# Kernel tuning notes

Measured on AMD Instinct MI355X. Metric: run time of the kernel, lower is better.

Reference implementation:

```python
import jax, jax.numpy as jnp
import numpy as np

PI = jnp.pi
NB_FRAMES = 2


def _axis_angle_to_R(r):
    # r: [..., 3] axis-angle -> rotation matrix [..., 3, 3] (Rodrigues)
    eps = 1e-8
    theta = jnp.sqrt(jnp.sum(r * r, axis=-1, keepdims=True))  # [...,1]
    k = r / jnp.maximum(theta, eps)
    kx, ky, kz = k[..., 0], k[..., 1], k[..., 2]
    zero = jnp.zeros_like(kx)
    K = jnp.stack([
        jnp.stack([zero, -kz, ky], axis=-1),
        jnp.stack([kz, zero, -kx], axis=-1),
        jnp.stack([-ky, kx, zero], axis=-1),
    ], axis=-2)  # [...,3,3]
    I = jnp.eye(3, dtype=r.dtype)
    s = jnp.sin(theta)[..., None]
    c = jnp.cos(theta)[..., None]
    return I + s * K + (1.0 - c) * (K @ K)


def _equirec_dirs(h, w, dtype):
    # unit viewing directions of an equirectangular grid, [h, w, 3]
    lon = ((jnp.arange(w, dtype=dtype) + 0.5) / w * 2.0 - 1.0) * PI
    lat = -((jnp.arange(h, dtype=dtype) + 0.5) / h * 2.0 - 1.0) * (0.5 * PI)
    LON, LAT = jnp.meshgrid(lon, lat)  # [h, w]
    dx = jnp.cos(LAT) * jnp.sin(LON)
    dy = jnp.sin(LAT)
    dz = jnp.cos(LAT) * jnp.cos(LON)
    return jnp.stack([dx, dy, dz], axis=-1)


def _grid_sample(img, grid):
    # img: [B,C,H,W]; grid: [B,Hg,Wg,2] in [-1,1] (x,y); bilinear,
    # align_corners=True, zero padding (matches F.grid_sample defaults)
    B, C, H, W = img.shape
    x = (grid[..., 0] + 1.0) * 0.5 * (W - 1)
    y = (grid[..., 1] + 1.0) * 0.5 * (H - 1)
    x0 = jnp.floor(x)
    y0 = jnp.floor(y)
    x1 = x0 + 1.0
    y1 = y0 + 1.0
    img_flat = img.reshape(B, C, H * W)

    def gather(xi, yi):
        valid = (xi >= 0) & (xi <= W - 1) & (yi >= 0) & (yi <= H - 1)
        xc = jnp.clip(xi, 0, W - 1).astype(jnp.int32)
        yc = jnp.clip(yi, 0, H - 1).astype(jnp.int32)
        idx = (yc * W + xc).reshape(B, 1, -1)
        v = jnp.take_along_axis(img_flat, idx, axis=2).reshape(B, C, *xi.shape[1:])
        return v * valid[:, None].astype(img.dtype)

    wa = ((x1 - x) * (y1 - y))[:, None]
    wb = ((x1 - x) * (y - y0))[:, None]
    wc = ((x - x0) * (y1 - y))[:, None]
    wd = ((x - x0) * (y - y0))[:, None]
    return (gather(x0, y0) * wa + gather(x0, y1) * wb +
            gather(x1, y0) * wc + gather(x1, y1) * wd)


def _area_down(x, s):
    # F.interpolate(mode='area') with integer factor == average pooling
    if s == 1:
        return x
    B, C, H, W = x.shape
    return x.reshape(B, C, H // s, s, W // s, s).mean(axis=(3, 5))


def _photometric_loss(ref_rgb, depths, masks, tgts, pose):
    R = _axis_angle_to_R(pose[..., 3:])      # [B, nb, 3, 3]
    t = pose[..., :3]                         # [B, nb, 3]
    loss = jnp.zeros((), dtype=ref_rgb.dtype)
    for i, (d, m) in enumerate(zip(depths, masks)):
        s = 2 ** i
        h, w = d.shape[2], d.shape[3]
        rr = _area_down(ref_rgb, s)                       # [B,3,h,w]
        tg = [_area_down(tr, s) for tr in tgts]
        dirs = _equirec_dirs(h, w, ref_rgb.dtype)         # [h,w,3]
        xyz = d[:, 0, :, :, None] * dirs[None]            # [B,h,w,3]
        # pose transform: pts = R @ xyz + t  -> [B,h,w,nb,3]
        pts = jnp.einsum('bnij,bhwj->bhwni', R, xyz) + t[:, None, None]
        norm = jnp.sqrt(jnp.sum(pts * pts, axis=-1))
        lon = jnp.arctan2(pts[..., 0], pts[..., 2])
        lat = jnp.arcsin(jnp.clip(pts[..., 1] / jnp.maximum(norm, 1e-8), -1.0, 1.0))
        X = lon / PI                  # [B,h,w,nb]
        Y = lat / (0.5 * PI)
        for j in range(NB_FRAMES):
            coord = jnp.stack([X[..., j], Y[..., j]], axis=-1)  # [B,h,w,2]
            wf = _grid_sample(tg[j], coord)                     # [B,3,h,w]
            loss = loss + jnp.mean(m[:, j:j + 1] * jnp.abs(rr - wf))
    return loss


def setup_inputs() -> dict:
    key = jax.random.key(0)
    ks = jax.random.split(key, 16)
    B, H, W = 8, 512, 1024
    inp = {'ref_rgb': jax.random.uniform(ks[0], (B, 3, H, W), jnp.float32)}
    for i in range(4):
        h, w = H // (2 ** i), W // (2 ** i)
        inp[f'ref_depth{i}'] = jax.random.uniform(ks[1 + i], (B, 1, h, w), jnp.float32)
        inp[f'exp_mask{i}'] = jax.random.uniform(ks[5 + i], (B, NB_FRAMES, h, w), jnp.float32)
    inp['tgt_rgb0'] = jax.random.uniform(ks[9], (B, 3, H, W), jnp.float32)
    inp['tgt_rgb1'] = jax.random.uniform(ks[10], (B, 3, H, W), jnp.float32)
    inp['pose'] = jax.random.normal(ks[11], (B, NB_FRAMES, 6), jnp.float32)
    return inp


def reference(ref_rgb, ref_depth0, ref_depth1, ref_depth2, ref_depth3,
              exp_mask0, exp_mask1, exp_mask2, exp_mask3,
              tgt_rgb0, tgt_rgb1, pose):
    depths = [ref_depth0, ref_depth1, ref_depth2, ref_depth3]
    masks = [exp_mask0, exp_mask1, exp_mask2, exp_mask3]
    tgts = [tgt_rgb0, tgt_rgb1]
    return _photometric_loss(ref_rgb, depths, masks, tgts, pose)
```

## Files before the change

kernel.cpp:

```cpp
#include <hip/hip_runtime.h>
#include <hip/hip_fp16.h>
#include <math.h>

#define PI_F 3.14159265358979323846f

__device__ inline float fast_atan2f(float y, float x) {
    float ax = fabsf(x), ay = fabsf(y);
    float mx = fmaxf(ax, ay);
    float mn = fminf(ax, ay);
    float a = __fdividef(mn, fmaxf(mx, 1e-30f));
    float s = a * a;
    float r = fmaf(s, fmaf(s, fmaf(s, fmaf(s, fmaf(s, -0.01172120f, 0.05265332f),
                   -0.11643287f), 0.19354346f), -0.33262347f), 0.99997726f);
    r = r * a;
    if (ay > ax) r = 1.57079632679f - r;
    if (x < 0.0f) r = PI_F - r;
    return copysignf(r, y);
}

__device__ inline void make_Rt_to(const float* __restrict__ pose, int bn, float* __restrict__ o) {
    const float* p = pose + bn * 6;
    float tx = p[0], ty = p[1], tz = p[2];
    float rx = p[3], ry = p[4], rz = p[5];
    float theta = sqrtf(rx * rx + ry * ry + rz * rz);
    float inv = __fdividef(1.0f, fmaxf(theta, 1e-8f));
    float kx = rx * inv, ky = ry * inv, kz = rz * inv;
    float s, c;
    __sincosf(theta, &s, &c);
    float oc = 1.0f - c;
    o[0] = 1.0f - oc * (ky * ky + kz * kz);
    o[1] = -s * kz + oc * kx * ky;
    o[2] =  s * ky + oc * kx * kz;
    o[3] =  s * kz + oc * kx * ky;
    o[4] = 1.0f - oc * (kx * kx + kz * kz);
    o[5] = -s * kx + oc * ky * kz;
    o[6] = -s * ky + oc * kx * kz;
    o[7] =  s * kx + oc * ky * kz;
    o[8] = 1.0f - oc * (kx * kx + ky * ky);
    o[9] = tx; o[10] = ty; o[11] = tz;
}

__device__ inline uint2 pack_px(float r, float g, float b) {
    __half2 a = __floats2half2_rn(r, g);
    __half2 c = __floats2half2_rn(b, 0.0f);
    uint2 u;
    u.x = *(const unsigned int*)&a;
    u.y = *(const unsigned int*)&c;
    return u;
}
__device__ inline float3 unpack_px(uint2 u) {
    __half2 a = *(const __half2*)&u.x;
    __half2 c = *(const __half2*)&u.y;
    float2 f = __half22float2(a);
    return make_float3(f.x, f.y, __low2float(c));
}

__global__ __launch_bounds__(256) void prep_kernel(
    const float* __restrict__ ref, const float* __restrict__ tgt0, const float* __restrict__ tgt1,
    uint2* __restrict__ packF,
    uint2* __restrict__ pL1t, uint2* __restrict__ pL2t, uint2* __restrict__ pL3t,
    uint2* __restrict__ pL1r, uint2* __restrict__ pL2r, uint2* __restrict__ pL3r)
{
    int bid = blockIdx.x;
    int band = bid & 63;
    int ib = bid >> 6;
    int b = ib & 7;
    int i = ib >> 3;
    const float* img = (i == 0) ? ref : (i == 1) ? tgt0 : tgt1;
    int t = threadIdx.x;
    int x4 = t << 2;
    int y0 = band << 3;
    int q = (i - 1) * 8 + b;

    float l1v[4][2][3];
#pragma unroll
    for (int p = 0; p < 4; ++p) {
        float4 a[3], bb[3];
#pragma unroll
        for (int c = 0; c < 3; ++c) {
            const float* pl = img + ((size_t)(b * 3 + c) << 19);
            a[c]  = *(const float4*)(pl + ((y0 + 2 * p) << 10) + x4);
            bb[c] = *(const float4*)(pl + ((y0 + 2 * p + 1) << 10) + x4);
        }
        if (i > 0) {
            uint2* o = packF + ((size_t)q << 19) + ((y0 + 2 * p) << 10) + x4;
            uint2 p0 = pack_px(a[0].x, a[1].x, a[2].x);
            uint2 p1 = pack_px(a[0].y, a[1].y, a[2].y);
            uint2 p2 = pack_px(a[0].z, a[1].z, a[2].z);
            uint2 p3 = pack_px(a[0].w, a[1].w, a[2].w);
            uint4 v0; v0.x = p0.x; v0.y = p0.y; v0.z = p1.x; v0.w = p1.y;
            uint4 v1; v1.x = p2.x; v1.y = p2.y; v1.z = p3.x; v1.w = p3.y;
            *(uint4*)o = v0;
            *(uint4*)(o + 2) = v1;
            uint2* o2 = o + (1 << 10);
            p0 = pack_px(bb[0].x, bb[1].x, bb[2].x);
            p1 = pack_px(bb[0].y, bb[1].y, bb[2].y);
            p2 = pack_px(bb[0].z, bb[1].z, bb[2].z);
            p3 = pack_px(bb[0].w, bb[1].w, bb[2].w);
            v0.x = p0.x; v0.y = p0.y; v0.z = p1.x; v0.w = p1.y;
            v1.x = p2.x; v1.y = p2.y; v1.z = p3.x; v1.w = p3.y;
            *(uint4*)o2 = v0;
            *(uint4*)(o2 + 2) = v1;
        }
#pragma unroll
        for (int c = 0; c < 3; ++c) {
            l1v[p][0][c] = (a[c].x + a[c].y + bb[c].x + bb[c].y) * 0.25f;
            l1v[p][1][c] = (a[c].z + a[c].w + bb[c].z + bb[c].w) * 0.25f;
        }
        uint2 q0 = pack_px(l1v[p][0][0], l1v[p][0][1], l1v[p][0][2]);
        uint2 q1 = pack_px(l1v[p][1][0], l1v[p][1][1], l1v[p][1][2]);
        uint4 v; v.x = q0.x; v.y = q0.y; v.z = q1.x; v.w = q1.y;
        uint2* d1 = ((i == 0) ? pL1r + ((size_t)b << 17) : pL1t + ((size_t)q << 17))
                    + (((band << 2) + p) << 9) + (t << 1);
        *(uint4*)d1 = v;
    }
    float l2v[2][3];
#pragma unroll
    for (int pr = 0; pr < 2; ++pr) {
#pragma unroll
        for (int c = 0; c < 3; ++c)
            l2v[pr][c] = (l1v[2 * pr][0][c] + l1v[2 * pr][1][c] +
                          l1v[2 * pr + 1][0][c] + l1v[2 * pr + 1][1][c]) * 0.25f;
        uint2* d2 = ((i == 0) ? pL2r + ((size_t)b << 15) : pL2t + ((size_t)q << 15))
                    + (((band << 1) + pr) << 8) + t;
        *d2 = pack_px(l2v[pr][0], l2v[pr][1], l2v[pr][2]);
    }
    float l3[3];
#pragma unroll
    for (int c = 0; c < 3; ++c) {
        float s = l2v[0][c] + l2v[1][c];
        l3[c] = (s + __shfl_xor(s, 1)) * 0.25f;
    }
    if ((t & 1) == 0) {
        uint2* d3 = ((i == 0) ? pL3r + ((size_t)b << 13) : pL3t + ((size_t)q << 13))
                    + (band << 7) + (t >> 1);
        *d3 = pack_px(l3[0], l3[1], l3[2]);
    }
}

template <int SH>
__device__ inline float photo_scale4(int bidl, int tid,
                                     const float* __restrict__ rrF,
                                     const uint2* __restrict__ rrP,
                                     const float* __restrict__ depth,
                                     const float* __restrict__ mask,
                                     const uint2* __restrict__ tg,
                                     const float* __restrict__ pose,
                                     float* __restrict__ ldsRt) {
    constexpr int h = 512 >> SH;
    constexpr int w = 1024 >> SH;
    constexpr int LOG2W = 10 - SH;
    constexpr int LP = 19 - 2 * SH;
    constexpr float inv_count = 1.0f / (8.0f * 3.0f * h * w);

    int lidx = ((bidl << 8) + tid) << 2;
    int b = lidx >> LP;
    if (tid < 2) make_Rt_to(pose, b * 2 + tid, ldsRt + tid * 12);
    __syncthreads();

    int x0 = lidx & (w - 1);
    int y = (lidx >> LOG2W) & (h - 1);
    int pix = (y << LOG2W) + x0;

    float lat = -(((float)y + 0.5f) * (2.0f / (float)h) - 1.0f) * (0.5f * PI_F);
    float slat = __sinf(lat), clat = __cosf(lat);

    float4 dep4 = *(const float4*)(depth + ((size_t)b << LP) + pix);
    float dp[4] = {dep4.x, dep4.y, dep4.z, dep4.w};
    float rcv[4][3];
    if constexpr (SH == 0) {
#pragma unroll
        for (int c = 0; c < 3; ++c) {
            float4 rv = *(const float4*)(rrF + ((size_t)(b * 3 + c) << LP) + pix);
            rcv[0][c] = rv.x; rcv[1][c] = rv.y; rcv[2][c] = rv.z; rcv[3][c] = rv.w;
        }
    } else {
        const uint2* rp = rrP + ((size_t)b << LP) + pix;
        uint4 u01 = *(const uint4*)rp;
        uint4 u23 = *(const uint4*)(rp + 2);
        uint2 e0; e0.x = u01.x; e0.y = u01.y;
        uint2 e1; e1.x = u01.z; e1.y = u01.w;
        uint2 e2; e2.x = u23.x; e2.y = u23.y;
        uint2 e3; e3.x = u23.z; e3.y = u23.w;
        float3 f0 = unpack_px(e0), f1 = unpack_px(e1), f2 = unpack_px(e2), f3 = unpack_px(e3);
        rcv[0][0] = f0.x; rcv[0][1] = f0.y; rcv[0][2] = f0.z;
        rcv[1][0] = f1.x; rcv[1][1] = f1.y; rcv[1][2] = f1.z;
        rcv[2][0] = f2.x; rcv[2][1] = f2.y; rcv[2][2] = f2.z;
        rcv[3][0] = f3.x; rcv[3][1] = f3.y; rcv[3][2] = f3.z;
    }
    float m4[2][4];
#pragma unroll
    for (int n = 0; n < 2; ++n) {
        float4 mv = *(const float4*)(mask + ((size_t)(b * 2 + n) << LP) + pix);
        m4[n][0] = mv.x; m4[n][1] = mv.y; m4[n][2] = mv.z; m4[n][3] = mv.w;
    }

    float acc = 0.0f;
#pragma unroll
    for (int i = 0; i < 4; ++i) {
        float lon = (((float)(x0 + i) + 0.5f) * (2.0f / (float)w) - 1.0f) * PI_F;
        float sl = __sinf(lon), cl = __cosf(lon);
        float X = dp[i] * clat * sl, Y = dp[i] * slat, Z = dp[i] * clat * cl;
#pragma unroll
        for (int n = 0; n < 2; ++n) {
            const float* R = ldsRt + n * 12;
            float px = R[0] * X + R[1] * Y + R[2] * Z + R[9];
            float py = R[3] * X + R[4] * Y + R[5] * Z + R[10];
            float pz = R[6] * X + R[7] * Y + R[8] * Z + R[11];
            float rxz = sqrtf(px * px + pz * pz);
            float lon2 = fast_atan2f(px, pz);
            float lat2 = fast_atan2f(py, rxz);
            float gx = (lon2 * (1.0f / PI_F) + 1.0f) * 0.5f * (float)(w - 1);
            float gy = (lat2 * (2.0f / PI_F) + 1.0f) * 0.5f * (float)(h - 1);
            float x0f = floorf(gx), y0f = floorf(gy);
            float fx = gx - x0f, fy = gy - y0f;
            float wa = (1.0f - fx) * (1.0f - fy);
            float wb = (1.0f - fx) * fy;
            float wc = fx * (1.0f - fy);
            float wd = fx * fy;
            bool vx0 = (x0f >= 0.0f) && (x0f <= (float)(w - 1));
            bool vx1 = (x0f >= -1.0f) && (x0f <= (float)(w - 2));
            bool vy0 = (y0f >= 0.0f) && (y0f <= (float)(h - 1));
            bool vy1 = (y0f >= -1.0f) && (y0f <= (float)(h - 2));
            int xi0 = (int)fminf(fmaxf(x0f, 0.0f), (float)(w - 1));
            int xi1 = (int)fminf(fmaxf(x0f + 1.0f, 0.0f), (float)(w - 1));
            int yi0 = (int)fminf(fmaxf(y0f, 0.0f), (float)(h - 1));
            int yi1 = (int)fminf(fmaxf(y0f + 1.0f, 0.0f), (float)(h - 1));
            float waf = (vx0 && vy0) ? wa : 0.0f;
            float wbf = (vx0 && vy1) ? wb : 0.0f;
            float wcf = (vx1 && vy0) ? wc : 0.0f;
            float wdf = (vx1 && vy1) ? wd : 0.0f;

            const uint2* plane = tg + ((size_t)(n * 8 + b) << LP);
            uint2 ua = plane[(yi0 << LOG2W) + xi0];
            uint2 ub = plane[(yi1 << LOG2W) + xi0];
            uint2 uc = plane[(yi0 << LOG2W) + xi1];
            uint2 ud = plane[(yi1 << LOG2W) + xi1];
            float3 ta = unpack_px(ua), tb = unpack_px(ub), tc = unpack_px(uc), td = unpack_px(ud);

            float m = m4[n][i];
            float v0 = waf * ta.x + wbf * tb.x + wcf * tc.x + wdf * td.x;
            float v1 = waf * ta.y + wbf * tb.y + wcf * tc.y + wdf * td.y;
            float v2 = waf * ta.z + wbf * tb.z + wcf * tc.z + wdf * td.z;
            acc += m * (fabsf(rcv[i][0] - v0) + fabsf(rcv[i][1] - v1) + fabsf(rcv[i][2] - v2));
        }
    }
    return acc * inv_count;
}

__global__ __launch_bounds__(256) void photo_all_packed4(
    const float* __restrict__ rrF,
    const uint2* __restrict__ rr1, const uint2* __restrict__ rr2, const uint2* __restrict__ rr3,
    const float* __restrict__ dep0, const float* __restrict__ msk0,
    const float* __restrict__ dep1, const float* __restrict__ msk1,
    const float* __restrict__ dep2, const float* __restrict__ msk2,
    const float* __restrict__ dep3, const float* __restrict__ msk3,
    const uint2* __restrict__ packF,
    const uint2* __restrict__ pL1t, const uint2* __restrict__ pL2t, const uint2* __restrict__ pL3t,
    const float* __restrict__ pose, float* __restrict__ out) {
    __shared__ float ldsRt[24];
    __shared__ float wsum[4];
    int bid = blockIdx.x, tid = threadIdx.x;
    float acc;
    if (bid < 4096)
        acc = photo_scale4<0>(bid, tid, rrF, nullptr, dep0, msk0, packF, pose, ldsRt);
    else if (bid < 5120)
        acc = photo_scale4<1>(bid - 4096, tid, nullptr, rr1, dep1, msk1, pL1t, pose, ldsRt);
    else if (bid < 5376)
        acc = photo_scale4<2>(bid - 5120, tid, nullptr, rr2, dep2, msk2, pL2t, pose, ldsRt);
    else
        acc = photo_scale4<3>(bid - 5376, tid, nullptr, rr3, dep3, msk3, pL3t, pose, ldsRt);

    for (int off = 32; off > 0; off >>= 1) acc += __shfl_down(acc, off);
    if ((tid & 63) == 0) wsum[tid >> 6] = acc;
    __syncthreads();
    if (tid == 0) atomicAdd(out, wsum[0] + wsum[1] + wsum[2] + wsum[3]);
}

template <int LWD>
__global__ __launch_bounds__(256) void down3_kernel(const float* __restrict__ sA,
                                                    const float* __restrict__ sB,
                                                    const float* __restrict__ sC,
                                                    float* __restrict__ dA,
                                                    float* __restrict__ dB,
                                                    float* __restrict__ dC) {
    const float* src = (blockIdx.y == 0) ? sA : (blockIdx.y == 1) ? sB : sC;
    float* dst = (blockIdx.y == 0) ? dA : (blockIdx.y == 1) ? dB : dC;
    int idx = blockIdx.x * 256 + threadIdx.x;
    constexpr int HB = LWD - 1;
    int xp = idx & ((1 << HB) - 1);
    int y = (idx >> HB) & ((1 << HB) - 1);
    int c = idx >> (2 * HB);
    const float* sp = src + ((size_t)c << (2 * LWD + 1)) + ((size_t)(2 * y) << (LWD + 1)) + 4 * xp;
    float4 r0 = *(const float4*)sp;
    float4 r1 = *(const float4*)(sp + (1 << (LWD + 1)));
    float2 d;
    d.x = 0.25f * (r0.x + r0.y + r1.x + r1.y);
    d.y = 0.25f * (r0.z + r0.w + r1.z + r1.w);
    *(float2*)(dst + ((size_t)c << (2 * LWD - 1)) + ((size_t)y << LWD) + 2 * xp) = d;
}

template <int SH>
__device__ inline float photo_scale(int bidl, int tid,
                                    const float* __restrict__ rr,
                                    const float* __restrict__ depth,
                                    const float* __restrict__ mask,
                                    const float* __restrict__ tg0,
                                    const float* __restrict__ tg1,
                                    const float* __restrict__ pose,
                                    float* __restrict__ ldsRt) {
    constexpr int h = 512 >> SH;
    constexpr int w = 1024 >> SH;
    constexpr int LOG2W = 10 - SH;
    constexpr int LP = 19 - 2 * SH;
    constexpr float inv_count = 1.0f / (8.0f * 3.0f * h * w);
    int lidx = (bidl << 8) + tid;
    int b = lidx >> LP;
    if (tid < 2) make_Rt_to(pose, b * 2 + tid, ldsRt + tid * 12);
    __syncthreads();
    int x = lidx & (w - 1);
    int y = (lidx >> LOG2W) & (h - 1);
    int pix = (y << LOG2W) + x;
    float lon = (((float)x + 0.5f) * (2.0f / (float)w) - 1.0f) * PI_F;
    float lat = -(((float)y + 0.5f) * (2.0f / (float)h) - 1.0f) * (0.5f * PI_F);
    float sl = __sinf(lon), cl = __cosf(lon);
    float slat = __sinf(lat), clat = __cosf(lat);
    float dep = depth[((size_t)b << LP) + pix];
    float X = dep * clat * sl, Y = dep * slat, Z = dep * clat * cl;
    float rc[3];
#pragma unroll
    for (int c = 0; c < 3; ++c)
        rc[c] = rr[((size_t)(b * 3 + c) << LP) + pix];
    float acc = 0.0f;
#pragma unroll
    for (int n = 0; n < 2; ++n) {
        const float* R = ldsRt + n * 12;
        float px = R[0] * X + R[1] * Y + R[2] * Z + R[9];
        float py = R[3] * X + R[4] * Y + R[5] * Z + R[10];
        float pz = R[6] * X + R[7] * Y + R[8] * Z + R[11];
        float rxz = sqrtf(px * px + pz * pz);
        float lon2 = fast_atan2f(px, pz);
        float lat2 = fast_atan2f(py, rxz);
        float gx = (lon2 * (1.0f / PI_F) + 1.0f) * 0.5f * (float)(w - 1);
        float gy = (lat2 * (2.0f / PI_F) + 1.0f) * 0.5f * (float)(h - 1);
        float x0f = floorf(gx), y0f = floorf(gy);
        float fx = gx - x0f, fy = gy - y0f;
        float wa = (1.0f - fx) * (1.0f - fy);
        float wb = (1.0f - fx) * fy;
        float wc = fx * (1.0f - fy);
        float wd = fx * fy;
        bool vx0 = (x0f >= 0.0f) && (x0f <= (float)(w - 1));
        bool vx1 = (x0f >= -1.0f) && (x0f <= (float)(w - 2));
        bool vy0 = (y0f >= 0.0f) && (y0f <= (float)(h - 1));
        bool vy1 = (y0f >= -1.0f) && (y0f <= (float)(h - 2));
        int xi0 = (int)fminf(fmaxf(x0f, 0.0f), (float)(w - 1));
        int xi1 = (int)fminf(fmaxf(x0f + 1.0f, 0.0f), (float)(w - 1));
        int yi0 = (int)fminf(fmaxf(y0f, 0.0f), (float)(h - 1));
        int yi1 = (int)fminf(fmaxf(y0f + 1.0f, 0.0f), (float)(h - 1));
        float waf = (vx0 && vy0) ? wa : 0.0f;
        float wbf = (vx0 && vy1) ? wb : 0.0f;
        float wcf = (vx1 && vy0) ? wc : 0.0f;
        float wdf = (vx1 && vy1) ? wd : 0.0f;
        int ia = (yi0 << LOG2W) + xi0;
        int ib2 = (yi1 << LOG2W) + xi0;
        int ic = (yi0 << LOG2W) + xi1;
        int id = (yi1 << LOG2W) + xi1;
        const float* tg = (n == 0) ? tg0 : tg1;
        float m = mask[((size_t)(b * 2 + n) << LP) + pix];
#pragma unroll
        for (int c = 0; c < 3; ++c) {
            const float* plane = tg + ((size_t)(b * 3 + c) << LP);
            float v = waf * plane[ia] + wbf * plane[ib2] + wcf * plane[ic] + wdf * plane[id];
            acc += m * fabsf(rc[c] - v);
        }
    }
    return acc * inv_count;
}

__global__ __launch_bounds__(256) void photo_all_kernel(
    const float* __restrict__ rr0, const float* __restrict__ dep0, const float* __restrict__ msk0,
    const float* __restrict__ tA0, const float* __restrict__ tB0,
    const float* __restrict__ rr1, const float* __restrict__ dep1, const float* __restrict__ msk1,
    const float* __restrict__ tA1, const float* __restrict__ tB1,
    const float* __restrict__ rr2, const float* __restrict__ dep2, const float* __restrict__ msk2,
    const float* __restrict__ tA2, const float* __restrict__ tB2,
    const float* __restrict__ rr3, const float* __restrict__ dep3, const float* __restrict__ msk3,
    const float* __restrict__ tA3, const float* __restrict__ tB3,
    const float* __restrict__ pose, float* __restrict__ out) {
    __shared__ float ldsRt[24];
    __shared__ float wsum[4];
    int bid = blockIdx.x, tid = threadIdx.x;
    float acc;
    if (bid < 16384)
        acc = photo_scale<0>(bid, tid, rr0, dep0, msk0, tA0, tB0, pose, ldsRt);
    else if (bid < 20480)
        acc = photo_scale<1>(bid - 16384, tid, rr1, dep1, msk1, tA1, tB1, pose, ldsRt);
    else if (bid < 21504)
        acc = photo_scale<2>(bid - 20480, tid, rr2, dep2, msk2, tA2, tB2, pose, ldsRt);
    else
        acc = photo_scale<3>(bid - 21504, tid, rr3, dep3, msk3, tA3, tB3, pose, ldsRt);
    for (int off = 32; off > 0; off >>= 1) acc += __shfl_down(acc, off);
    if ((tid & 63) == 0) wsum[tid >> 6] = acc;
    __syncthreads();
    if (tid == 0) atomicAdd(out, wsum[0] + wsum[1] + wsum[2] + wsum[3]);
}

extern "C" void kernel_launch(void* const* d_in, const int* in_sizes, int n_in,
                              void* d_out, int out_size, void* d_ws, size_t ws_size,
                              hipStream_t stream) {
    const float* ref  = (const float*)d_in[0];
    const float* dep0 = (const float*)d_in[1];
    const float* msk0 = (const float*)d_in[2];
    const float* dep1 = (const float*)d_in[3];
    const float* msk1 = (const float*)d_in[4];
    const float* dep2 = (const float*)d_in[5];
    const float* msk2 = (const float*)d_in[6];
    const float* dep3 = (const float*)d_in[7];
    const float* msk3 = (const float*)d_in[8];
    const float* tgt0 = (const float*)d_in[9];
    const float* tgt1 = (const float*)d_in[10];
    const float* pose = (const float*)d_in[11];
    float* out = (float*)d_out;

    hipMemsetAsync(out, 0, sizeof(float), stream);

    const size_t E_F   = (size_t)16 << 19;
    const size_t E_L1t = (size_t)16 << 17;
    const size_t E_L2t = (size_t)16 << 15;
    const size_t E_L3t = (size_t)16 << 13;
    const size_t E_L1r = (size_t)8 << 17;
    const size_t E_L2r = (size_t)8 << 15;
    const size_t E_L3r = (size_t)8 << 13;
    const size_t NEED_PACKED = (E_F + E_L1t + E_L2t + E_L3t + E_L1r + E_L2r + E_L3r) * sizeof(uint2);

    const size_t L1 = (size_t)24 * 256 * 512;
    const size_t L2 = (size_t)24 * 128 * 256;
    const size_t L3 = (size_t)24 * 64 * 128;
    const size_t NEED_A = 3 * (L1 + L2 + L3) * sizeof(float);

    if (ws_size >= NEED_PACKED) {
        uint2* p = (uint2*)d_ws;
        uint2* packF = p; p += E_F;
        uint2* pL1t = p; p += E_L1t;
        uint2* pL2t = p; p += E_L2t;
        uint2* pL3t = p; p += E_L3t;
        uint2* pL1r = p; p += E_L1r;
        uint2* pL2r = p; p += E_L2r;
        uint2* pL3r = p; p += E_L3r;

        prep_kernel<<<1536, 256, 0, stream>>>(ref, tgt0, tgt1, packF,
                                              pL1t, pL2t, pL3t, pL1r, pL2r, pL3r);
        photo_all_packed4<<<5440, 256, 0, stream>>>(
            ref, pL1r, pL2r, pL3r,
            dep0, msk0, dep1, msk1, dep2, msk2, dep3, msk3,
            packF, pL1t, pL2t, pL3t, pose, out);
    } else if (ws_size >= NEED_A) {
        float* p = (float*)d_ws;
        float* ref_l1 = p; p += L1;
        float* ref_l2 = p; p += L2;
        float* ref_l3 = p; p += L3;
        float* t0_l1 = p; p += L1;
        float* t0_l2 = p; p += L2;
        float* t0_l3 = p; p += L3;
        float* t1_l1 = p; p += L1;
        float* t1_l2 = p; p += L2;
        float* t1_l3 = p; p += L3;
        down3_kernel<9><<<dim3((24 << 16) / 256, 3), 256, 0, stream>>>(
            ref, tgt0, tgt1, ref_l1, t0_l1, t1_l1);
        down3_kernel<8><<<dim3((24 << 14) / 256, 3), 256, 0, stream>>>(
            ref_l1, t0_l1, t1_l1, ref_l2, t0_l2, t1_l2);
        down3_kernel<7><<<dim3((24 << 12) / 256, 3), 256, 0, stream>>>(
            ref_l2, t0_l2, t1_l2, ref_l3, t0_l3, t1_l3);
        photo_all_kernel<<<21760, 256, 0, stream>>>(
            ref, dep0, msk0, tgt0, tgt1,
            ref_l1, dep1, msk1, t0_l1, t1_l1,
            ref_l2, dep2, msk2, t0_l2, t1_l2,
            ref_l3, dep3, msk3, t0_l3, t1_l3,
            pose, out);
    }
}
```

Measured before the change: 357.6 us.

## Batch gather loads, swizzle block order, fold memset into prep kernel

The photometric kernel now computes all 32 bilinear tap offsets and weights first, issues every gather load together, and only then blends. This exposes more memory-level parallelism. Block indices in both kernels are remapped so that consecutive blocks touch different batches or images, which spreads the load across L2/MALL channels. The separate memset of the output is removed and the zeroing is done by thread 0 of the prep kernel, saving one launch. The cost is higher register pressure from holding 32 taps, which may lower occupancy.

```diff
diff --git a/kernel.cpp b/kernel.cpp
--- a/kernel.cpp
+++ b/kernel.cpp
@@ -59,15 +59,17 @@
     const float* __restrict__ ref, const float* __restrict__ tgt0, const float* __restrict__ tgt1,
     uint2* __restrict__ packF,
     uint2* __restrict__ pL1t, uint2* __restrict__ pL2t, uint2* __restrict__ pL3t,
-    uint2* __restrict__ pL1r, uint2* __restrict__ pL2r, uint2* __restrict__ pL3r)
+    uint2* __restrict__ pL1r, uint2* __restrict__ pL2r, uint2* __restrict__ pL3r,
+    float* __restrict__ out)
 {
     int bid = blockIdx.x;
-    int band = bid & 63;
-    int ib = bid >> 6;
-    int b = ib & 7;
-    int i = ib >> 3;
+    int t = threadIdx.x;
+    if (bid == 0 && t == 0) out[0] = 0.0f;
+    int i = bid % 3;
+    int rem = bid / 3;
+    int b = rem & 7;
+    int band = rem >> 3;
     const float* img = (i == 0) ? ref : (i == 1) ? tgt0 : tgt1;
-    int t = threadIdx.x;
     int x4 = t << 2;
     int y0 = band << 3;
     int q = (i - 1) * 8 + b;
@@ -195,7 +197,11 @@
         m4[n][0] = mv.x; m4[n][1] = mv.y; m4[n][2] = mv.z; m4[n][3] = mv.w;
     }
 
-    float acc = 0.0f;
+    const uint2* pl0 = tg + ((size_t)b << LP);
+    const uint2* pl1 = tg + ((size_t)(8 + b) << LP);
+
+    float wt[8][4];
+    int off[8][4];
 #pragma unroll
     for (int i = 0; i < 4; ++i) {
         float lon = (((float)(x0 + i) + 0.5f) * (2.0f / (float)w) - 1.0f) * PI_F;
@@ -226,24 +232,36 @@
             int xi1 = (int)fminf(fmaxf(x0f + 1.0f, 0.0f), (float)(w - 1));
             int yi0 = (int)fminf(fmaxf(y0f, 0.0f), (float)(h - 1));
             int yi1 = (int)fminf(fmaxf(y0f + 1.0f, 0.0f), (float)(h - 1));
-            float waf = (vx0 && vy0) ? wa : 0.0f;
-            float wbf = (vx0 && vy1) ? wb : 0.0f;
-            float wcf = (vx1 && vy0) ? wc : 0.0f;
-            float wdf = (vx1 && vy1) ? wd : 0.0f;
-
-            const uint2* plane = tg + ((size_t)(n * 8 + b) << LP);
-            uint2 ua = plane[(yi0 << LOG2W) + xi0];
-            uint2 ub = plane[(yi1 << LOG2W) + xi0];
-            uint2 uc = plane[(yi0 << LOG2W) + xi1];
-            uint2 ud = plane[(yi1 << LOG2W) + xi1];
-            float3 ta = unpack_px(ua), tb = unpack_px(ub), tc = unpack_px(uc), td = unpack_px(ud);
-
-            float m = m4[n][i];
-            float v0 = waf * ta.x + wbf * tb.x + wcf * tc.x + wdf * td.x;
-            float v1 = waf * ta.y + wbf * tb.y + wcf * tc.y + wdf * td.y;
-            float v2 = waf * ta.z + wbf * tb.z + wcf * tc.z + wdf * td.z;
-            acc += m * (fabsf(rcv[i][0] - v0) + fabsf(rcv[i][1] - v1) + fabsf(rcv[i][2] - v2));
+            int g = i * 2 + n;
+            wt[g][0] = (vx0 && vy0) ? wa : 0.0f;
+            wt[g][1] = (vx0 && vy1) ? wb : 0.0f;
+            wt[g][2] = (vx1 && vy0) ? wc : 0.0f;
+            wt[g][3] = (vx1 && vy1) ? wd : 0.0f;
+            off[g][0] = (yi0 << LOG2W) + xi0;
+            off[g][1] = (yi1 << LOG2W) + xi0;
+            off[g][2] = (yi0 << LOG2W) + xi1;
+            off[g][3] = (yi1 << LOG2W) + xi1;
         }
+    }
+    uint2 tap[8][4];
+#pragma unroll
+    for (int g = 0; g < 8; ++g) {
+        const uint2* P = (g & 1) ? pl1 : pl0;
+#pragma unroll
+        for (int k = 0; k < 4; ++k) tap[g][k] = P[off[g][k]];
+    }
+    float acc = 0.0f;
+#pragma unroll
+    for (int g = 0; g < 8; ++g) {
+        int i = g >> 1, n = g & 1;
+        float3 ta = unpack_px(tap[g][0]);
+        float3 tb = unpack_px(tap[g][1]);
+        float3 tc = unpack_px(tap[g][2]);
+        float3 td = unpack_px(tap[g][3]);
+        float v0 = wt[g][0] * ta.x + wt[g][1] * tb.x + wt[g][2] * tc.x + wt[g][3] * td.x;
+        float v1 = wt[g][0] * ta.y + wt[g][1] * tb.y + wt[g][2] * tc.y + wt[g][3] * td.y;
+        float v2 = wt[g][0] * ta.z + wt[g][1] * tb.z + wt[g][2] * tc.z + wt[g][3] * td.z;
+        acc += m4[n][i] * (fabsf(rcv[i][0] - v0) + fabsf(rcv[i][1] - v1) + fabsf(rcv[i][2] - v2));
     }
     return acc * inv_count;
 }
@@ -262,14 +280,22 @@
     __shared__ float wsum[4];
     int bid = blockIdx.x, tid = threadIdx.x;
     float acc;
-    if (bid < 4096)
-        acc = photo_scale4<0>(bid, tid, rrF, nullptr, dep0, msk0, packF, pose, ldsRt);
-    else if (bid < 5120)
-        acc = photo_scale4<1>(bid - 4096, tid, nullptr, rr1, dep1, msk1, pL1t, pose, ldsRt);
-    else if (bid < 5376)
-        acc = photo_scale4<2>(bid - 5120, tid, nullptr, rr2, dep2, msk2, pL2t, pose, ldsRt);
-    else
-        acc = photo_scale4<3>(bid - 5376, tid, nullptr, rr3, dep3, msk3, pL3t, pose, ldsRt);
+    if (bid < 4096) {
+        int s = ((bid & 7) << 9) | (bid >> 3);
+        acc = photo_scale4<0>(s, tid, rrF, nullptr, dep0, msk0, packF, pose, ldsRt);
+    } else if (bid < 5120) {
+        int t0 = bid - 4096;
+        int s = ((t0 & 7) << 7) | (t0 >> 3);
+        acc = photo_scale4<1>(s, tid, nullptr, rr1, dep1, msk1, pL1t, pose, ldsRt);
+    } else if (bid < 5376) {
+        int t0 = bid - 5120;
+        int s = ((t0 & 7) << 5) | (t0 >> 3);
+        acc = photo_scale4<2>(s, tid, nullptr, rr2, dep2, msk2, pL2t, pose, ldsRt);
+    } else {
+        int t0 = bid - 5376;
+        int s = ((t0 & 7) << 3) | (t0 >> 3);
+        acc = photo_scale4<3>(s, tid, nullptr, rr3, dep3, msk3, pL3t, pose, ldsRt);
+    }
 
     for (int off = 32; off > 0; off >>= 1) acc += __shfl_down(acc, off);
     if ((tid & 63) == 0) wsum[tid >> 6] = acc;
@@ -422,8 +448,6 @@
     const float* pose = (const float*)d_in[11];
     float* out = (float*)d_out;
 
-    hipMemsetAsync(out, 0, sizeof(float), stream);
-
     const size_t E_F   = (size_t)16 << 19;
     const size_t E_L1t = (size_t)16 << 17;
     const size_t E_L2t = (size_t)16 << 15;
@@ -449,12 +473,13 @@
         uint2* pL3r = p; p += E_L3r;
 
         prep_kernel<<<1536, 256, 0, stream>>>(ref, tgt0, tgt1, packF,
-                                              pL1t, pL2t, pL3t, pL1r, pL2r, pL3r);
+                                              pL1t, pL2t, pL3t, pL1r, pL2r, pL3r, out);
         photo_all_packed4<<<5440, 256, 0, stream>>>(
             ref, pL1r, pL2r, pL3r,
             dep0, msk0, dep1, msk1, dep2, msk2, dep3, msk3,
             packF, pL1t, pL2t, pL3t, pose, out);
     } else if (ws_size >= NEED_A) {
+        hipMemsetAsync(out, 0, sizeof(float), stream);
         float* p = (float*)d_ws;
         float* ref_l1 = p; p += L1;
         float* ref_l2 = p; p += L2;
```

After: 349.6 us. -2.3%, faster.
